# Kernel optimization log

Hardware: AMD Instinct MI355X
Metric: run time of the kernel (lower is better)

## Reference

```python
import jax, jax.numpy as jnp
from jax import lax
import numpy as np

B, T, D_IN = 1024, 64, 1662
H1, H2, H3 = 64, 128, 64


def _lstm_layer(x, w_ih, w_hh, b_ih, b_hh):
    """PyTorch-convention single-layer LSTM. x: [B,T,D]; gate order i,f,g,o."""
    Bc = x.shape[0]
    H = w_hh.shape[1]
    # Precompute input contribution for all timesteps: [B,T,4H]
    xg = jnp.einsum('btd,gd->btg', x, w_ih) + b_ih + b_hh

    def step(carry, xt):
        h, c = carry
        gates = xt + h @ w_hh.T  # [B,4H]
        i, f, g, o = jnp.split(gates, 4, axis=-1)
        i = jax.nn.sigmoid(i)
        f = jax.nn.sigmoid(f)
        g = jnp.tanh(g)
        o = jax.nn.sigmoid(o)
        c = f * c + i * g
        h = o * jnp.tanh(c)
        return (h, c), h

    h0 = jnp.zeros((Bc, H), x.dtype)
    (_, _), hs = lax.scan(step, (h0, h0), jnp.swapaxes(xg, 0, 1))
    return jnp.swapaxes(hs, 0, 1)  # [B,T,H]


def setup_inputs() -> dict:
    key = jax.random.key(0)
    ks = jax.random.split(key, 20)

    def u(k, shape, fan):
        bound = 1.0 / np.sqrt(fan)
        return jax.random.uniform(k, shape, jnp.float32, -bound, bound)

    x = jax.random.normal(ks[0], (B, T, D_IN), jnp.float32)
    return {
        'x': x,
        'w_ih1': u(ks[1], (4 * H1, D_IN), H1), 'w_hh1': u(ks[2], (4 * H1, H1), H1),
        'b_ih1': u(ks[3], (4 * H1,), H1),      'b_hh1': u(ks[4], (4 * H1,), H1),
        'w_ih2': u(ks[5], (4 * H2, H1), H2),   'w_hh2': u(ks[6], (4 * H2, H2), H2),
        'b_ih2': u(ks[7], (4 * H2,), H2),      'b_hh2': u(ks[8], (4 * H2,), H2),
        'w_ih3': u(ks[9], (4 * H3, H2), H3),   'w_hh3': u(ks[10], (4 * H3, H3), H3),
        'b_ih3': u(ks[11], (4 * H3,), H3),     'b_hh3': u(ks[12], (4 * H3,), H3),
        'fc1_w': u(ks[13], (64, 64), 64),      'fc1_b': u(ks[14], (64,), 64),
        'fc2_w': u(ks[15], (32, 64), 64),      'fc2_b': u(ks[16], (32,), 64),
        'fc3_w': u(ks[17], (3, 32), 32),       'fc3_b': u(ks[18], (3,), 32),
    }


def reference(x, w_ih1, w_hh1, b_ih1, b_hh1,
              w_ih2, w_hh2, b_ih2, b_hh2,
              w_ih3, w_hh3, b_ih3, b_hh3,
              fc1_w, fc1_b, fc2_w, fc2_b, fc3_w, fc3_b):
    h = _lstm_layer(x, w_ih1, w_hh1, b_ih1, b_hh1)   # [B,T,64]
    h = _lstm_layer(h, w_ih2, w_hh2, b_ih2, b_hh2)   # [B,T,128]
    h = _lstm_layer(h, w_ih3, w_hh3, b_ih3, b_hh3)   # [B,T,64]
    h = h[:, -1, :]                                   # [B,64]
    h = jax.nn.relu(h @ fc1_w.T + fc1_b)
    h = jax.nn.relu(h @ fc2_w.T + fc2_b)
    return jax.nn.softmax(h @ fc3_w.T + fc3_b, axis=1)  # [B,3]
```

## Files before the change

kernel.cpp:

```cpp
#include <hip/hip_runtime.h>
#include <hip/hip_bf16.h>

#define B_SZ   1024
#define T_SZ   64
#define D_IN   1662
#define D_INP  1664
#define M_SZ   (B_SZ * T_SZ)

typedef __attribute__((ext_vector_type(8))) short short8;
typedef __attribute__((ext_vector_type(4))) float f32x4;
typedef unsigned short ushort_t;

__device__ __forceinline__ unsigned short f2bf(float f) {
    unsigned u = __builtin_bit_cast(unsigned, f);
    u += 0x7FFFu + ((u >> 16) & 1u);
    return (unsigned short)(u >> 16);
}
__device__ __forceinline__ float bf2f(ushort_t u) {
    return __builtin_bit_cast(float, (unsigned)u << 16);
}

#define GLD16(gp, lp) __builtin_amdgcn_global_load_lds(                        \
    (const __attribute__((address_space(1))) void*)(gp),                       \
    (__attribute__((address_space(3))) void*)(lp), 16, 0, 0)

__device__ __forceinline__ float sigmoid_f(float x) {
    return 1.0f / (1.0f + __expf(-x));
}
__device__ __forceinline__ float tanh_f(float x) {
    float a = fabsf(x);
    float e = __expf(2.0f * a);
    float r = 1.0f - 2.0f / (e + 1.0f);
    return copysignf(r, x);
}

__global__ __launch_bounds__(256) void convert_w1(
    const float* __restrict__ src, ushort_t* __restrict__ dst)
{
    constexpr int cpr = D_INP >> 3;
    const int total = 256 * cpr;
    const int stride = gridDim.x * blockDim.x;
    for (int idx = blockIdx.x * blockDim.x + threadIdx.x;
         idx < total; idx += stride) {
        const int row  = idx / cpr;
        const int base = (idx % cpr) << 3;
        const float* s = src + (size_t)row * D_IN;
        short8 o;
        #pragma unroll
        for (int j = 0; j < 4; ++j) {
            const int k = base + 2 * j;
            float2 v = make_float2(0.f, 0.f);
            if (k < D_IN) v = *(const float2*)(s + k);
            o[2 * j]     = (short)f2bf(v.x);
            o[2 * j + 1] = (short)f2bf(v.y);
        }
        *(short8*)(dst + (size_t)row * D_INP + base) = o;
    }
}

__global__ __launch_bounds__(256, 4) void gemm_l1(
    const float* __restrict__ A, const ushort_t* __restrict__ W,
    ushort_t* __restrict__ out)
{
    constexpr int K = D_IN, Kp = D_INP, G = 256;
    __shared__ __align__(16) ushort_t As[64 * 32];
    __shared__ __align__(16) ushort_t Ws[256 * 32];

    const int tid = threadIdx.x, lane = tid & 63, wid = tid >> 6;
    const int m0 = blockIdx.x * 64;

    const int arow  = tid >> 2;
    const int acolb = (tid & 3) * 8;
    const float* Abase = A + (size_t)(m0 + arow) * K + acolb;

    const size_t wlofs = (size_t)(lane >> 2) * Kp + (lane & 3) * 8;
    const ushort_t* Wg0 = W + (size_t)(wid * 64) * Kp + wlofs;
    const ushort_t* Wg1 = Wg0 + (size_t)16 * Kp;
    const ushort_t* Wg2 = Wg0 + (size_t)32 * Kp;
    const ushort_t* Wg3 = Wg0 + (size_t)48 * Kp;
    ushort_t* lw0 = &Ws[(wid * 64) * 32];
    ushort_t* lw1 = lw0 + 16 * 32;
    ushort_t* lw2 = lw0 + 32 * 32;
    ushort_t* lw3 = lw0 + 48 * 32;

    const int fr = lane & 15, kq = (lane >> 4) * 8;

    f32x4 acc[4][4] = {};
    const int nFull = K / 32;

    float2 av[4];
    #pragma unroll
    for (int j = 0; j < 4; ++j) av[j] = *(const float2*)(Abase + 2 * j);

    for (int it = 0; it <= nFull; ++it) {
        const int k0 = it * 32;
        __syncthreads();
        GLD16(Wg0 + k0, lw0); GLD16(Wg1 + k0, lw1);
        GLD16(Wg2 + k0, lw2); GLD16(Wg3 + k0, lw3);
        short8 pk;
        #pragma unroll
        for (int j = 0; j < 4; ++j) {
            pk[2 * j]     = (short)f2bf(av[j].x);
            pk[2 * j + 1] = (short)f2bf(av[j].y);
        }
        *(short8*)&As[arow * 32 + acolb] = pk;
        __syncthreads();

        if (it < nFull) {
            const int kn = (it + 1) * 32;
            if (it + 1 < nFull) {
                #pragma unroll
                for (int j = 0; j < 4; ++j)
                    av[j] = *(const float2*)(Abase + kn + 2 * j);
            } else {
                #pragma unroll
                for (int j = 0; j < 4; ++j) {
                    const int kk = kn + acolb + 2 * j;
                    av[j] = (kk < K) ? *(const float2*)(Abase + kn + 2 * j)
                                     : make_float2(0.f, 0.f);
                }
            }
        }

        short8 af[4], bfr[4];
        #pragma unroll
        for (int fm = 0; fm < 4; ++fm)
            af[fm] = *(const short8*)&As[(fm * 16 + fr) * 32 + kq];
        #pragma unroll
        for (int fn = 0; fn < 4; ++fn)
            bfr[fn] = *(const short8*)&Ws[(wid * 64 + fn * 16 + fr) * 32 + kq];
        #pragma unroll
        for (int fm = 0; fm < 4; ++fm)
            #pragma unroll
            for (int fn = 0; fn < 4; ++fn)
                acc[fm][fn] = __builtin_amdgcn_mfma_f32_16x16x32_bf16(
                    af[fm], bfr[fn], acc[fm][fn], 0, 0, 0);
    }

    const int rbase = (lane >> 4) * 4;
    #pragma unroll
    for (int fn = 0; fn < 4; ++fn) {
        const int g = wid * 64 + fn * 16 + fr;
        #pragma unroll
        for (int fm = 0; fm < 4; ++fm) {
            const int mbase = m0 + fm * 16 + rbase;
            #pragma unroll
            for (int j = 0; j < 4; ++j)
                out[(size_t)(mbase + j) * G + g] = f2bf(acc[fm][fn][j]);
        }
    }
}

__global__ __launch_bounds__(512, 1) void lstm3_pipe(
    const ushort_t* __restrict__ xg1,
    const float* __restrict__ whh1,
    const float* __restrict__ bih1, const float* __restrict__ bhh1,
    const float* __restrict__ wih2, const float* __restrict__ whh2,
    const float* __restrict__ bih2, const float* __restrict__ bhh2,
    const float* __restrict__ wih3, const float* __restrict__ whh3,
    const float* __restrict__ bih3, const float* __restrict__ bhh3,
    float* __restrict__ hlast, int Tn)
{
    __shared__ ushort_t h1sh[2][16 * 64];
    __shared__ ushort_t h2sh[2][16 * 128];
    __shared__ ushort_t h3sh[2][16 * 64];
    __shared__ ushort_t xsh[2][4 * 256];
    __shared__ float    gsh[4][1024];
    __shared__ float    bsh[1024];

    const int tid = threadIdx.x, lane = tid & 63, wid = tid >> 6;
    const int r0 = blockIdx.x * 4;
    const int fr = lane & 15, hi = lane >> 4, kq = hi * 8;

    int role, uw;
    if (wid < 2)      { role = 1; uw = wid * 32; }
    else if (wid < 6) { role = 2; uw = (wid - 2) * 32; }
    else              { role = 3; uw = (wid - 6) * 32; }

    short8 bregB[2][4][2];
    short8 bregA[2][4][4];
    #pragma unroll
    for (int ut = 0; ut < 2; ++ut)
        #pragma unroll
        for (int g = 0; g < 4; ++g) {
            const int uu = uw + ut * 16 + fr;
            const float *pB, *pA = nullptr;
            if (role == 1)      { pB = whh1 + (size_t)(g * 64 + uu) * 64; }
            else if (role == 2) { pB = wih2 + (size_t)(g * 128 + uu) * 64;
                                  pA = whh2 + (size_t)(g * 128 + uu) * 128; }
            else                { pB = whh3 + (size_t)(g * 64 + uu) * 64;
                                  pA = wih3 + (size_t)(g * 64 + uu) * 128; }
            #pragma unroll
            for (int ks = 0; ks < 2; ++ks) {
                short8 b;
                #pragma unroll
                for (int j = 0; j < 8; ++j)
                    b[j] = (short)f2bf(pB[ks * 32 + kq + j]);
                bregB[ut][g][ks] = b;
            }
            if (role >= 2) {
                #pragma unroll
                for (int ks = 0; ks < 4; ++ks) {
                    short8 b;
                    #pragma unroll
                    for (int j = 0; j < 8; ++j)
                        b[j] = (short)f2bf(pA[ks * 32 + kq + j]);
                    bregA[ut][g][ks] = b;
                }
            }
        }

    for (int i = tid; i < 1024; i += 512) {
        float bv;
        if (i < 256)      bv = bih1[i] + bhh1[i];
        else if (i < 768) bv = bih2[i - 256] + bhh2[i - 256];
        else              bv = bih3[i - 768] + bhh3[i - 768];
        bsh[i] = bv;
        h1sh[0][i] = 0; h1sh[1][i] = 0;
        h3sh[0][i] = 0; h3sh[1][i] = 0;
    }
    for (int i = tid; i < 2048; i += 512) { h2sh[0][i] = 0; h2sh[1][i] = 0; }

    if (tid < 128) {
        const int rw = tid >> 5, xc = (tid & 31) * 8;
        *(short8*)&xsh[0][rw * 256 + xc] =
            *(const short8*)(xg1 + ((size_t)(r0 + rw) * Tn) * 256 + xc);
    }

    float c[2] = {0.f, 0.f};
    __syncthreads();

    const int nSteps = Tn + 2;
    for (int s = 0; s < nSteps; ++s) {
        const int rb = s & 1, wb = rb ^ 1;

        short8 xr;
        const bool doX = (tid < 128) && (s + 1 < Tn);
        if (doX) {
            const int rw = tid >> 5, xc = (tid & 31) * 8;
            xr = *(const short8*)(xg1 +
                 ((size_t)(r0 + rw) * Tn + (s + 1)) * 256 + xc);
        }

        const bool act = (role == 1) ? (s < Tn)
                       : (role == 2) ? (s >= 1 && s <= Tn)
                                     : (s >= 2 && s <= Tn + 1);
        if (act) {
            short8 a2r[2], a4r[4];
            const ushort_t* src2 = (role == 3) ? h3sh[rb] : h1sh[rb];
            #pragma unroll
            for (int ks = 0; ks < 2; ++ks) {
                const int k0 = ks * 32 + kq;
                a2r[ks] = *(const short8*)&src2[fr * 64 + (k0 ^ ((fr & 7) << 3))];
            }
            if (role >= 2) {
                #pragma unroll
                for (int ks = 0; ks < 4; ++ks) {
                    const int k0 = ks * 32 + kq;
                    a4r[ks] = *(const short8*)
                        &h2sh[rb][fr * 128 + (k0 ^ ((fr & 7) << 3))];
                }
            }
            const int sec = (role == 1) ? 0 : (role == 2) ? 256 : 768;
            const int Hl  = (role == 2) ? 128 : 64;
            #pragma unroll
            for (int ut = 0; ut < 2; ++ut)
                #pragma unroll
                for (int g = 0; g < 4; ++g) {
                    f32x4 acc = {};
                    #pragma unroll
                    for (int ks = 0; ks < 2; ++ks)
                        acc = __builtin_amdgcn_mfma_f32_16x16x32_bf16(
                            a2r[ks], bregB[ut][g][ks], acc, 0, 0, 0);
                    if (role >= 2) {
                        #pragma unroll
                        for (int ks = 0; ks < 4; ++ks)
                            acc = __builtin_amdgcn_mfma_f32_16x16x32_bf16(
                                a4r[ks], bregA[ut][g][ks], acc, 0, 0, 0);
                    }
                    if (hi == 0) {
                        const int col = sec + g * Hl + uw + ut * 16 + fr;
                        #pragma unroll
                        for (int j = 0; j < 4; ++j)
                            gsh[j][col] = acc[j];
                    }
                }
        }
        __syncthreads();

        #pragma unroll
        for (int i = 0; i < 2; ++i) {
            const int item = tid + i * 512;
            const int row = item >> 8, ug = item & 255;
            int u, Hl, sec, tt, lay;
            if (ug < 64)       { lay = 1; u = ug;       Hl = 64;  sec = 0;   tt = s; }
            else if (ug < 192) { lay = 2; u = ug - 64;  Hl = 128; sec = 256; tt = s - 1; }
            else               { lay = 3; u = ug - 192; Hl = 64;  sec = 768; tt = s - 2; }
            if (tt >= 0 && tt < Tn) {
                const int col0 = sec + u;
                float gi = gsh[row][col0]          + bsh[col0];
                float gf = gsh[row][col0 + Hl]     + bsh[col0 + Hl];
                float gg = gsh[row][col0 + 2 * Hl] + bsh[col0 + 2 * Hl];
                float go = gsh[row][col0 + 3 * Hl] + bsh[col0 + 3 * Hl];
                if (lay == 1) {
                    const ushort_t* xb = &xsh[s & 1][row * 256 + u];
                    gi += bf2f(xb[0]);   gf += bf2f(xb[64]);
                    gg += bf2f(xb[128]); go += bf2f(xb[192]);
                }
                const float iv = sigmoid_f(gi);
                const float fv = sigmoid_f(gf);
                const float gv = tanh_f(gg);
                const float ov = sigmoid_f(go);
                c[i] = fmaf(fv, c[i], iv * gv);
                const float h = ov * tanh_f(c[i]);
                ushort_t* hdst = (lay == 1) ? h1sh[wb]
                               : (lay == 2) ? h2sh[wb] : h3sh[wb];
                hdst[row * Hl + (u ^ (row << 3))] = f2bf(h);
                if (lay == 3 && tt == Tn - 1)
                    hlast[(size_t)(r0 + row) * 64 + u] = h;
            }
        }

        if (doX) {
            const int rw = tid >> 5, xc = (tid & 31) * 8;
            *(short8*)&xsh[(s + 1) & 1][rw * 256 + xc] = xr;
        }
        __syncthreads();
    }
}

__global__ __launch_bounds__(256) void head_kernel(
    const float* __restrict__ hlast,
    const float* __restrict__ w1, const float* __restrict__ b1,
    const float* __restrict__ w2, const float* __restrict__ b2,
    const float* __restrict__ w3, const float* __restrict__ b3,
    float* __restrict__ out)
{
    __shared__ float W1[64][64];
    __shared__ float W2[32][64];
    __shared__ float W3[3][32];
    __shared__ float hin[16][64];
    __shared__ float a1[16][64];
    __shared__ float a2[16][32];
    __shared__ float lg[16][3];

    const int tid = threadIdx.x;
    const int r0 = blockIdx.x * 16;

    for (int i = tid; i < 64 * 64; i += 256) W1[i >> 6][i & 63] = w1[i];
    for (int i = tid; i < 32 * 64; i += 256) W2[i >> 6][i & 63] = w2[i];
    for (int i = tid; i < 3 * 32; i += 256) W3[i >> 5][i & 31] = w3[i];
    for (int i = tid; i < 16 * 64; i += 256) {
        int r = i >> 6, u = i & 63;
        hin[r][u] = hlast[(size_t)(r0 + r) * 64 + u];
    }
    __syncthreads();

    for (int i = tid; i < 16 * 64; i += 256) {
        int r = i >> 6, j = i & 63;
        float s = b1[j];
        #pragma unroll
        for (int k = 0; k < 64; ++k) s = fmaf(hin[r][k], W1[j][k], s);
        a1[r][j] = fmaxf(s, 0.f);
    }
    __syncthreads();

    for (int i = tid; i < 16 * 32; i += 256) {
        int r = i >> 5, j = i & 31;
        float s = b2[j];
        #pragma unroll
        for (int k = 0; k < 64; ++k) s = fmaf(a1[r][k], W2[j][k], s);
        a2[r][j] = fmaxf(s, 0.f);
    }
    __syncthreads();

    for (int i = tid; i < 16 * 3; i += 256) {
        int r = i / 3, j = i % 3;
        float s = b3[j];
        #pragma unroll
        for (int k = 0; k < 32; ++k) s = fmaf(a2[r][k], W3[j][k], s);
        lg[r][j] = s;
    }
    __syncthreads();

    if (tid < 16) {
        float l0 = lg[tid][0], l1 = lg[tid][1], l2 = lg[tid][2];
        float m = fmaxf(l0, fmaxf(l1, l2));
        float e0 = __expf(l0 - m), e1 = __expf(l1 - m), e2 = __expf(l2 - m);
        float inv = 1.0f / (e0 + e1 + e2);
        out[(size_t)(r0 + tid) * 3 + 0] = e0 * inv;
        out[(size_t)(r0 + tid) * 3 + 1] = e1 * inv;
        out[(size_t)(r0 + tid) * 3 + 2] = e2 * inv;
    }
}

extern "C" void kernel_launch(void* const* d_in, const int* in_sizes, int n_in,
                              void* d_out, int out_size, void* d_ws, size_t ws_size,
                              hipStream_t stream)
{
    const float* x    = (const float*)d_in[0];
    const float* wih1 = (const float*)d_in[1];
    const float* whh1 = (const float*)d_in[2];
    const float* bih1 = (const float*)d_in[3];
    const float* bhh1 = (const float*)d_in[4];
    const float* wih2 = (const float*)d_in[5];
    const float* whh2 = (const float*)d_in[6];
    const float* bih2 = (const float*)d_in[7];
    const float* bhh2 = (const float*)d_in[8];
    const float* wih3 = (const float*)d_in[9];
    const float* whh3 = (const float*)d_in[10];
    const float* bih3 = (const float*)d_in[11];
    const float* bhh3 = (const float*)d_in[12];
    const float* f1w  = (const float*)d_in[13];
    const float* f1b  = (const float*)d_in[14];
    const float* f2w  = (const float*)d_in[15];
    const float* f2b  = (const float*)d_in[16];
    const float* f3w  = (const float*)d_in[17];
    const float* f3b  = (const float*)d_in[18];
    float* outp = (float*)d_out;

    char* wsb = (char*)d_ws;
    size_t off = 0;
    ushort_t* bufA  = (ushort_t*)(wsb + off); off += 33554432;
    float*    hlast = (float*)(wsb + off);    off += 262144;
    ushort_t* w1b   = (ushort_t*)(wsb + off);

    const int T = T_SZ;

    convert_w1<<<208, 256, 0, stream>>>(wih1, w1b);

    gemm_l1<<<M_SZ / 64, 256, 0, stream>>>(x, w1b, bufA);

    lstm3_pipe<<<B_SZ / 4, 512, 0, stream>>>(
        bufA, whh1, bih1, bhh1,
        wih2, whh2, bih2, bhh2,
        wih3, whh3, bih3, bhh3,
        hlast, T);

    head_kernel<<<B_SZ / 16, 256, 0, stream>>>(
        hlast, f1w, f1b, f2w, f2b, f3w, f3b, outp);
}
```

Before: 371.7 us.

## Fuse LSTM cell update into owning wave, drop mid-step barrier

Each wave now writes its gate pre-activations to a private per-wave shared buffer and applies the LSTM cell update to its own units. This removes one block-wide barrier per timestep and the cross-wave redistribution through a shared gate array. Biases are kept in registers, the next-step x slice is fetched with an asynchronous global-to-LDS load, weights are read as float4, and launch bounds allow two blocks per CU. The intra-wave LDS write-then-read relies on wave-level ordering, and the async x load has to complete before the next step's barrier.

Result: faster. 356.3 us (-4.1%).

```diff
diff --git a/kernel.cpp b/kernel.cpp
--- a/kernel.cpp
+++ b/kernel.cpp
@@ -151,7 +151,7 @@
     }
 }
 
-__global__ __launch_bounds__(512, 1) void lstm3_pipe(
+__global__ __launch_bounds__(512, 2) void lstm3_gg(
     const ushort_t* __restrict__ xg1,
     const float* __restrict__ whh1,
     const float* __restrict__ bih1, const float* __restrict__ bhh1,
@@ -164,62 +164,75 @@
     __shared__ ushort_t h1sh[2][16 * 64];
     __shared__ ushort_t h2sh[2][16 * 128];
     __shared__ ushort_t h3sh[2][16 * 64];
-    __shared__ ushort_t xsh[2][4 * 256];
-    __shared__ float    gsh[4][1024];
-    __shared__ float    bsh[1024];
+    __shared__ __align__(16) ushort_t xsh[2][1024];
+    __shared__ __align__(16) float gsw[8][128 * 4];
 
     const int tid = threadIdx.x, lane = tid & 63, wid = tid >> 6;
     const int r0 = blockIdx.x * 4;
     const int fr = lane & 15, hi = lane >> 4, kq = hi * 8;
 
-    int role, uw;
-    if (wid < 2)      { role = 1; uw = wid * 32; }
-    else if (wid < 6) { role = 2; uw = (wid - 2) * 32; }
-    else              { role = 3; uw = (wid - 6) * 32; }
-
-    short8 bregB[2][4][2];
-    short8 bregA[2][4][4];
+    int role, ubase, Hl;
+    if (wid < 2)      { role = 1; ubase = wid * 32;       Hl = 64; }
+    else if (wid < 6) { role = 2; ubase = (wid - 2) * 32; Hl = 128; }
+    else              { role = 3; ubase = (wid - 6) * 32; Hl = 64; }
+
+    short8 bregS[2][4][2];
+    short8 bregL[2][4][4];
     #pragma unroll
     for (int ut = 0; ut < 2; ++ut)
         #pragma unroll
         for (int g = 0; g < 4; ++g) {
-            const int uu = uw + ut * 16 + fr;
-            const float *pB, *pA = nullptr;
-            if (role == 1)      { pB = whh1 + (size_t)(g * 64 + uu) * 64; }
-            else if (role == 2) { pB = wih2 + (size_t)(g * 128 + uu) * 64;
-                                  pA = whh2 + (size_t)(g * 128 + uu) * 128; }
-            else                { pB = whh3 + (size_t)(g * 64 + uu) * 64;
-                                  pA = wih3 + (size_t)(g * 64 + uu) * 128; }
+            const int uu = ubase + ut * 16 + fr;
+            const float *pS, *pL = nullptr;
+            if (role == 1)      { pS = whh1 + (size_t)(g * 64 + uu) * 64; }
+            else if (role == 2) { pS = wih2 + (size_t)(g * 128 + uu) * 64;
+                                  pL = whh2 + (size_t)(g * 128 + uu) * 128; }
+            else                { pS = whh3 + (size_t)(g * 64 + uu) * 64;
+                                  pL = wih3 + (size_t)(g * 64 + uu) * 128; }
             #pragma unroll
             for (int ks = 0; ks < 2; ++ks) {
+                const float4 v0 = *(const float4*)(pS + ks * 32 + kq);
+                const float4 v1 = *(const float4*)(pS + ks * 32 + kq + 4);
                 short8 b;
-                #pragma unroll
-                for (int j = 0; j < 8; ++j)
-                    b[j] = (short)f2bf(pB[ks * 32 + kq + j]);
-                bregB[ut][g][ks] = b;
+                b[0] = (short)f2bf(v0.x); b[1] = (short)f2bf(v0.y);
+                b[2] = (short)f2bf(v0.z); b[3] = (short)f2bf(v0.w);
+                b[4] = (short)f2bf(v1.x); b[5] = (short)f2bf(v1.y);
+                b[6] = (short)f2bf(v1.z); b[7] = (short)f2bf(v1.w);
+                bregS[ut][g][ks] = b;
             }
             if (role >= 2) {
                 #pragma unroll
                 for (int ks = 0; ks < 4; ++ks) {
+                    const float4 v0 = *(const float4*)(pL + ks * 32 + kq);
+                    const float4 v1 = *(const float4*)(pL + ks * 32 + kq + 4);
                     short8 b;
-                    #pragma unroll
-                    for (int j = 0; j < 8; ++j)
-                        b[j] = (short)f2bf(pA[ks * 32 + kq + j]);
-                    bregA[ut][g][ks] = b;
+                    b[0] = (short)f2bf(v0.x); b[1] = (short)f2bf(v0.y);
+                    b[2] = (short)f2bf(v0.z); b[3] = (short)f2bf(v0.w);
+                    b[4] = (short)f2bf(v1.x); b[5] = (short)f2bf(v1.y);
+                    b[6] = (short)f2bf(v1.z); b[7] = (short)f2bf(v1.w);
+                    bregL[ut][g][ks] = b;
                 }
             }
         }
 
-    for (int i = tid; i < 1024; i += 512) {
-        float bv;
-        if (i < 256)      bv = bih1[i] + bhh1[i];
-        else if (i < 768) bv = bih2[i - 256] + bhh2[i - 256];
-        else              bv = bih3[i - 768] + bhh3[i - 768];
-        bsh[i] = bv;
+    float bias[2][4];
+    {
+        const float* bihp = (role == 1) ? bih1 : (role == 2) ? bih2 : bih3;
+        const float* bhhp = (role == 1) ? bhh1 : (role == 2) ? bhh2 : bhh3;
+        #pragma unroll
+        for (int i = 0; i < 2; ++i) {
+            const int unit = ubase + i * 16 + fr;
+            #pragma unroll
+            for (int g = 0; g < 4; ++g)
+                bias[i][g] = bihp[g * Hl + unit] + bhhp[g * Hl + unit];
+        }
+    }
+
+    for (int i = tid; i < 16 * 64; i += 512) {
         h1sh[0][i] = 0; h1sh[1][i] = 0;
         h3sh[0][i] = 0; h3sh[1][i] = 0;
     }
-    for (int i = tid; i < 2048; i += 512) { h2sh[0][i] = 0; h2sh[1][i] = 0; }
+    for (int i = tid; i < 16 * 128; i += 512) { h2sh[0][i] = 0; h2sh[1][i] = 0; }
 
     if (tid < 128) {
         const int rw = tid >> 5, xc = (tid & 31) * 8;
@@ -234,35 +247,33 @@
     for (int s = 0; s < nSteps; ++s) {
         const int rb = s & 1, wb = rb ^ 1;
 
-        short8 xr;
-        const bool doX = (tid < 128) && (s + 1 < Tn);
-        if (doX) {
-            const int rw = tid >> 5, xc = (tid & 31) * 8;
-            xr = *(const short8*)(xg1 +
-                 ((size_t)(r0 + rw) * Tn + (s + 1)) * 256 + xc);
+        if (wid < 2 && s + 1 < Tn) {
+            const int rw = wid * 2 + (lane >> 5);
+            const int xc = (lane & 31) * 8;
+            GLD16(xg1 + ((size_t)(r0 + rw) * Tn + (s + 1)) * 256 + xc,
+                  &xsh[wb][wid * 512]);
         }
 
         const bool act = (role == 1) ? (s < Tn)
                        : (role == 2) ? (s >= 1 && s <= Tn)
                                      : (s >= 2 && s <= Tn + 1);
         if (act) {
-            short8 a2r[2], a4r[4];
-            const ushort_t* src2 = (role == 3) ? h3sh[rb] : h1sh[rb];
+            short8 aS[2], aL[4];
+            const ushort_t* srcS = (role == 3) ? h3sh[rb] : h1sh[rb];
             #pragma unroll
             for (int ks = 0; ks < 2; ++ks) {
                 const int k0 = ks * 32 + kq;
-                a2r[ks] = *(const short8*)&src2[fr * 64 + (k0 ^ ((fr & 7) << 3))];
+                aS[ks] = *(const short8*)&srcS[fr * 64 + (k0 ^ ((fr & 7) << 3))];
             }
             if (role >= 2) {
                 #pragma unroll
                 for (int ks = 0; ks < 4; ++ks) {
                     const int k0 = ks * 32 + kq;
-                    a4r[ks] = *(const short8*)
+                    aL[ks] = *(const short8*)
                         &h2sh[rb][fr * 128 + (k0 ^ ((fr & 7) << 3))];
                 }
             }
-            const int sec = (role == 1) ? 0 : (role == 2) ? 256 : 768;
-            const int Hl  = (role == 2) ? 128 : 64;
+
             #pragma unroll
             for (int ut = 0; ut < 2; ++ut)
                 #pragma unroll
@@ -271,39 +282,27 @@
                     #pragma unroll
                     for (int ks = 0; ks < 2; ++ks)
                         acc = __builtin_amdgcn_mfma_f32_16x16x32_bf16(
-                            a2r[ks], bregB[ut][g][ks], acc, 0, 0, 0);
+                            aS[ks], bregS[ut][g][ks], acc, 0, 0, 0);
                     if (role >= 2) {
                         #pragma unroll
                         for (int ks = 0; ks < 4; ++ks)
                             acc = __builtin_amdgcn_mfma_f32_16x16x32_bf16(
-                                a4r[ks], bregA[ut][g][ks], acc, 0, 0, 0);
+                                aL[ks], bregL[ut][g][ks], acc, 0, 0, 0);
                     }
-                    if (hi == 0) {
-                        const int col = sec + g * Hl + uw + ut * 16 + fr;
-                        #pragma unroll
-                        for (int j = 0; j < 4; ++j)
-                            gsh[j][col] = acc[j];
-                    }
+                    if (hi == 0)
+                        *(f32x4*)&gsw[wid][(g * 32 + ut * 16 + fr) * 4] = acc;
                 }
-        }
-        __syncthreads();
-
-        #pragma unroll
-        for (int i = 0; i < 2; ++i) {
-            const int item = tid + i * 512;
-            const int row = item >> 8, ug = item & 255;
-            int u, Hl, sec, tt, lay;
-            if (ug < 64)       { lay = 1; u = ug;       Hl = 64;  sec = 0;   tt = s; }
-            else if (ug < 192) { lay = 2; u = ug - 64;  Hl = 128; sec = 256; tt = s - 1; }
-            else               { lay = 3; u = ug - 192; Hl = 64;  sec = 768; tt = s - 2; }
-            if (tt >= 0 && tt < Tn) {
-                const int col0 = sec + u;
-                float gi = gsh[row][col0]          + bsh[col0];
-                float gf = gsh[row][col0 + Hl]     + bsh[col0 + Hl];
-                float gg = gsh[row][col0 + 2 * Hl] + bsh[col0 + 2 * Hl];
-                float go = gsh[row][col0 + 3 * Hl] + bsh[col0 + 3 * Hl];
-                if (lay == 1) {
-                    const ushort_t* xb = &xsh[s & 1][row * 256 + u];
+
+            #pragma unroll
+            for (int i = 0; i < 2; ++i) {
+                const int uloc = i * 16 + fr;
+                const int unit = ubase + uloc;
+                float gi = gsw[wid][(0 * 32 + uloc) * 4 + hi] + bias[i][0];
+                float gf = gsw[wid][(1 * 32 + uloc) * 4 + hi] + bias[i][1];
+                float gg = gsw[wid][(2 * 32 + uloc) * 4 + hi] + bias[i][2];
+                float go = gsw[wid][(3 * 32 + uloc) * 4 + hi] + bias[i][3];
+                if (role == 1) {
+                    const ushort_t* xb = &xsh[rb][hi * 256 + unit];
                     gi += bf2f(xb[0]);   gf += bf2f(xb[64]);
                     gg += bf2f(xb[128]); go += bf2f(xb[192]);
                 }
@@ -313,17 +312,12 @@
                 const float ov = sigmoid_f(go);
                 c[i] = fmaf(fv, c[i], iv * gv);
                 const float h = ov * tanh_f(c[i]);
-                ushort_t* hdst = (lay == 1) ? h1sh[wb]
-                               : (lay == 2) ? h2sh[wb] : h3sh[wb];
-                hdst[row * Hl + (u ^ (row << 3))] = f2bf(h);
-                if (lay == 3 && tt == Tn - 1)
-                    hlast[(size_t)(r0 + row) * 64 + u] = h;
-            }
-        }
-
-        if (doX) {
-            const int rw = tid >> 5, xc = (tid & 31) * 8;
-            *(short8*)&xsh[(s + 1) & 1][rw * 256 + xc] = xr;
+                ushort_t* hdst = (role == 1) ? h1sh[wb]
+                               : (role == 2) ? h2sh[wb] : h3sh[wb];
+                hdst[hi * Hl + (unit ^ (hi << 3))] = f2bf(h);
+                if (role == 3 && s == Tn + 1)
+                    hlast[(size_t)(r0 + hi) * 64 + unit] = h;
+            }
         }
         __syncthreads();
     }
@@ -431,7 +425,7 @@
 
     gemm_l1<<<M_SZ / 64, 256, 0, stream>>>(x, w1b, bufA);
 
-    lstm3_pipe<<<B_SZ / 4, 512, 0, stream>>>(
+    lstm3_gg<<<B_SZ / 4, 512, 0, stream>>>(
         bufA, whh1, bih1, bhh1,
         wih2, whh2, bih2, bhh2,
         wih3, whh3, bih3, bhh3,
```
